# Kernel optimization log

Hardware: AMD Instinct MI355X
Metric: run time of the kernel (lower is better)

The kernel has to match this reference:

```python
import jax, jax.numpy as jnp
import numpy as np

LOG_VAR_Q = 0.0
TEMPERATURE = 0.5


def setup_inputs() -> dict:
    key = jax.random.key(0)
    k1, k2, k3 = jax.random.split(key, 3)
    bs, dim_z, W, H, K = 64, 64, 32, 32, 1024
    x = jax.random.normal(k1, (bs, dim_z, W, H), dtype=jnp.float32)
    codebook = jax.random.normal(k2, (K, dim_z), dtype=jnp.float32)
    log_var_q_scalar = jnp.asarray(0.0, dtype=jnp.float32)
    # pre-sampled standard Gumbel noise for the relaxed categorical
    u = jax.random.uniform(k3, (bs * W * H, K), dtype=jnp.float32,
                           minval=1e-6, maxval=1.0 - 1e-6)
    gumbel_noise = -jnp.log(-jnp.log(u))
    return {"x": x, "codebook": codebook,
            "log_var_q_scalar": log_var_q_scalar,
            "gumbel_noise": gumbel_noise}


def reference(x, codebook, log_var_q_scalar, gumbel_noise):
    bs, dim_z, W, H = x.shape
    # [bs, dim_z, W, H] -> [bs*W*H, dim_z]
    x_flat = jnp.transpose(x, (0, 2, 3, 1)).reshape(-1, dim_z)

    var_q = jnp.exp(jnp.asarray(LOG_VAR_Q, x.dtype)) + jnp.exp(log_var_q_scalar)
    precision_q = 1.0 / jnp.clip(var_q, 1e-10)
    w = 0.5 * precision_q  # scalar weight on squared distances

    sq_x = jnp.sum(x_flat * x_flat, axis=-1, keepdims=True)
    sq_c = jnp.sum(codebook * codebook, axis=-1)
    cross = jnp.einsum('nd,kd->nk', x_flat, codebook)
    logit = -w * (sq_x - 2.0 * cross + sq_c)

    log_probs = jax.nn.log_softmax(logit, axis=-1)
    probs = jnp.exp(log_probs)

    # gumbel-softmax relaxed one-hot encodings
    encodings = jax.nn.softmax((logit + gumbel_noise) / TEMPERATURE, axis=-1)

    quantized = jnp.einsum('nk,kd->nd', encodings, codebook)
    quantized = jnp.transpose(quantized.reshape(bs, W, H, dim_z), (0, 3, 1, 2))

    kld_discrete = jnp.sum(probs * log_probs) / bs
    kld_continuous = jnp.mean(jnp.sum(w * (x - quantized) ** 2, axis=(1, 2, 3)))
    return quantized, kld_discrete + kld_continuous
```

## Files before the change

### kernel.cpp

```cpp
#include <hip/hip_runtime.h>
#include <math.h>

#define K_CB 1024
#define D_Z  64
#define MT   16
#define NTOT 65536
#define NBLK (NTOT / MT)

typedef __attribute__((ext_vector_type(8))) short  s16x8;
typedef __attribute__((ext_vector_type(4))) short  s16x4;
typedef __attribute__((ext_vector_type(4))) float  f32x4;

#define WS_CB16  0
#define WS_CBT16 131072
#define WS_NWSQC 262144
#define WS_PART  266240

__device__ __forceinline__ unsigned short f2b(float f) {
  unsigned int u = __float_as_uint(f);
  u += 0x7fffu + ((u >> 16) & 1u);
  return (unsigned short)(u >> 16);
}

__global__ void vq_prep(const float* __restrict__ cb, const float* __restrict__ lvq,
                        unsigned char* __restrict__ wsb) {
  unsigned short* cb16  = (unsigned short*)(wsb + WS_CB16);
  unsigned short* cbT16 = (unsigned short*)(wsb + WS_CBT16);
  float* nwsqc = (float*)(wsb + WS_NWSQC);
  const float w = 0.5f / fmaxf(1.0f + __expf(lvq[0]), 1e-10f);
  const int tid = threadIdx.x;
  const int k  = blockIdx.x * 16 + (tid >> 4);
  const int d0 = (tid & 15) * 4;
  const f32x4 v = *(const f32x4*)(cb + k * D_Z + d0);
  s16x4 b4;
  #pragma unroll
  for (int i = 0; i < 4; i++) b4[i] = (short)f2b(v[i]);
  *(s16x4*)(cb16 + k * D_Z + d0) = b4;
  #pragma unroll
  for (int i = 0; i < 4; i++) cbT16[(d0 + i) * K_CB + k] = (unsigned short)b4[i];
  float s = v[0]*v[0] + v[1]*v[1] + v[2]*v[2] + v[3]*v[3];
  #pragma unroll
  for (int off = 1; off < 16; off <<= 1) s += __shfl_xor(s, off);
  if ((tid & 15) == 0) nwsqc[k] = -w * s;
}

__global__ __launch_bounds__(256, 3)
void vq_main(const float* __restrict__ x, const float* __restrict__ gum,
             const float* __restrict__ lvq, unsigned char* __restrict__ wsb,
             float* __restrict__ out) {
  __shared__ __align__(16) unsigned short xa[1024];
  __shared__ __align__(16) float xs[MT][68];
  __shared__ __align__(16) float sqcs[K_CB];
  __shared__ __align__(16) unsigned short es[MT][1032];
  __shared__ __align__(16) float pstat[4][MT][4];
  __shared__ __align__(16) float s2p[4][MT];
  __shared__ float kldrow[MT];
  __shared__ float wred[4];

  const int tid  = threadIdx.x;
  const int wv   = tid >> 6;
  const int lane = tid & 63;
  const int m16  = lane & 15;
  const int g    = lane >> 4;

  const int blk  = blockIdx.x;
  const int row0 = blk * MT;
  const int bidx = row0 >> 10;
  const int rem0 = row0 & 1023;

  const float w  = 0.5f / fmaxf(1.0f + __expf(lvq[0]), 1e-10f);
  const float w2 = 2.0f * w;

  const unsigned short* cb16  = (const unsigned short*)(wsb + WS_CB16);
  const unsigned short* cbT16 = (const unsigned short*)(wsb + WS_CBT16);
  const float* nwsqc = (const float*)(wsb + WS_NWSQC);

  {
    const int m = tid & 15, db = tid >> 4;
    #pragma unroll
    for (int i = 0; i < 4; i++) {
      const int d = db + 16 * i;
      const float v = x[((bidx * D_Z + d) << 10) + rem0 + m];
      xs[m][d] = v;
      xa[(d >> 5) * 512 + ((d >> 3) & 3) * 128 + m * 8 + (d & 7)] = f2b(v);
    }
    for (int k = tid; k < K_CB; k += 256) sqcs[k] = nwsqc[k];
  }
  __syncthreads();

  f32x4 acc[16];
  #pragma unroll
  for (int t = 0; t < 16; t++) acc[t] = (f32x4){0.f, 0.f, 0.f, 0.f};
  {
    const s16x8 xb0 = *(const s16x8*)(xa + g * 128 + m16 * 8);
    const s16x8 xb1 = *(const s16x8*)(xa + 512 + g * 128 + m16 * 8);
    const unsigned short* ap = cb16 + (wv * 256 + m16) * D_Z + g * 8;
    #pragma unroll
    for (int t = 0; t < 16; t++) {
      const s16x8 a0 = *(const s16x8*)(ap + t * 1024);
      const s16x8 a1 = *(const s16x8*)(ap + t * 1024 + 32);
      acc[t] = __builtin_amdgcn_mfma_f32_16x16x32_bf16(a0, xb0, acc[t], 0, 0, 0);
      acc[t] = __builtin_amdgcn_mfma_f32_16x16x32_bf16(a1, xb1, acc[t], 0, 0, 0);
    }
  }

  float m1 = -3.4e38f;
  #pragma unroll
  for (int t = 0; t < 16; t++) {
    const f32x4 sc = *(const f32x4*)&sqcs[wv * 256 + t * 16 + g * 4];
    #pragma unroll
    for (int r = 0; r < 4; r++) {
      acc[t][r] = fmaf(w2, acc[t][r], sc[r]);
      m1 = fmaxf(m1, acc[t][r]);
    }
  }
  m1 = fmaxf(m1, __shfl_xor(m1, 16));
  m1 = fmaxf(m1, __shfl_xor(m1, 32));
  float s1 = 0.f, Aa = 0.f;
  #pragma unroll
  for (int t = 0; t < 16; t++) {
    #pragma unroll
    for (int r = 0; r < 4; r++) {
      const float u = acc[t][r] - m1;
      const float e = __expf(u);
      s1 += e;
      Aa = fmaf(u, e, Aa);
    }
  }
  s1 += __shfl_xor(s1, 16); s1 += __shfl_xor(s1, 32);
  Aa += __shfl_xor(Aa, 16); Aa += __shfl_xor(Aa, 32);

  float m2 = -3.4e38f;
  const float* gp = gum + (row0 + m16) * K_CB + wv * 256 + g * 4;
  #pragma unroll
  for (int t = 0; t < 16; t++) {
    const f32x4 gv = __builtin_nontemporal_load((const f32x4*)(gp + t * 16));
    #pragma unroll
    for (int r = 0; r < 4; r++) {
      const float z = 2.0f * (acc[t][r] + gv[r]);
      acc[t][r] = z;
      m2 = fmaxf(m2, z);
    }
  }
  m2 = fmaxf(m2, __shfl_xor(m2, 16));
  m2 = fmaxf(m2, __shfl_xor(m2, 32));
  if (g == 0) {
    pstat[wv][m16][0] = m1; pstat[wv][m16][1] = s1;
    pstat[wv][m16][2] = Aa; pstat[wv][m16][3] = m2;
  }
  __syncthreads();

  float M2 = -3.4e38f;
  {
    float M1 = -3.4e38f;
    f32x4 pw[4];
    #pragma unroll
    for (int q = 0; q < 4; q++) {
      pw[q] = *(const f32x4*)&pstat[q][m16][0];
      M1 = fmaxf(M1, pw[q][0]);
      M2 = fmaxf(M2, pw[q][3]);
    }
    float s1g = 0.f, Ag = 0.f;
    #pragma unroll
    for (int q = 0; q < 4; q++) {
      const float dm = pw[q][0] - M1;
      const float c = __expf(dm);
      s1g += c * pw[q][1];
      Ag = fmaf(c, fmaf(dm, pw[q][1], pw[q][2]), Ag);
    }
    if (tid < 16) kldrow[m16] = Ag / s1g - __logf(s1g);
  }

  float s2 = 0.f;
  #pragma unroll
  for (int t = 0; t < 16; t++) {
    s16x4 ev;
    #pragma unroll
    for (int r = 0; r < 4; r++) {
      const float e = __expf(acc[t][r] - M2);
      s2 += e;
      ev[r] = (short)f2b(e);
    }
    *(s16x4*)&es[m16][wv * 256 + t * 16 + g * 4] = ev;
  }
  s2 += __shfl_xor(s2, 16); s2 += __shfl_xor(s2, 32);
  if (g == 0) s2p[wv][m16] = s2;
  __syncthreads();

  const float inv2 = 1.0f / (s2p[0][m16] + s2p[1][m16] + s2p[2][m16] + s2p[3][m16]);
  f32x4 qacc = (f32x4){0.f, 0.f, 0.f, 0.f};
  {
    const unsigned short* a2p = cbT16 + (wv * 16 + m16) * K_CB + g * 8;
    const unsigned short* b2p = &es[m16][g * 8];
    #pragma unroll
    for (int kc = 0; kc < 32; kc++) {
      const s16x8 a2 = *(const s16x8*)(a2p + kc * 32);
      const s16x8 b2 = *(const s16x8*)(b2p + kc * 32);
      qacc = __builtin_amdgcn_mfma_f32_16x16x32_bf16(a2, b2, qacc, 0, 0, 0);
    }
  }

  float kca = 0.f;
  #pragma unroll
  for (int r = 0; r < 4; r++) {
    const int d = wv * 16 + g * 4 + r;
    const float qv = qacc[r] * inv2;
    __builtin_nontemporal_store(qv, out + ((bidx * D_Z + d) << 10) + rem0 + m16);
    const float dx = xs[m16][d] - qv;
    kca = fmaf(dx, dx, kca);
  }
  #pragma unroll
  for (int off = 1; off < 64; off <<= 1) kca += __shfl_xor(kca, off);
  if (lane == 0) wred[wv] = kca;
  __syncthreads();
  if (tid == 0) {
    float tot = w * (wred[0] + wred[1] + wred[2] + wred[3]);
    #pragma unroll
    for (int i = 0; i < MT; i++) tot += kldrow[i];
    ((float*)(wsb + WS_PART))[blk] = tot;
  }
}

__global__ void vq_reduce(const unsigned char* __restrict__ wsb, float* __restrict__ out) {
  __shared__ float red[256];
  const float* part = (const float*)(wsb + WS_PART);
  const int t = threadIdx.x;
  float s = 0.f;
  for (int i = t; i < NBLK; i += 256) s += part[i];
  red[t] = s;
  __syncthreads();
  for (int st = 128; st > 0; st >>= 1) {
    if (t < st) red[t] += red[t + st];
    __syncthreads();
  }
  if (t == 0) out[NTOT * D_Z] = red[0] * (1.0f / 64.0f);
}

extern "C" void kernel_launch(void* const* d_in, const int* in_sizes, int n_in,
                              void* d_out, int out_size, void* d_ws, size_t ws_size,
                              hipStream_t stream) {
  const float* x   = (const float*)d_in[0];
  const float* cb  = (const float*)d_in[1];
  const float* lvq = (const float*)d_in[2];
  const float* gum = (const float*)d_in[3];
  float* out = (float*)d_out;
  unsigned char* wsb = (unsigned char*)d_ws;

  hipLaunchKernelGGL(vq_prep,   dim3(64),   dim3(256), 0, stream, cb, lvq, wsb);
  hipLaunchKernelGGL(vq_main,   dim3(NBLK), dim3(256), 0, stream, x, gum, lvq, wsb, out);
  hipLaunchKernelGGL(vq_reduce, dim3(1),    dim3(256), 0, stream, wsb, out);
}
```

Baseline: 179.1 us.

## Drop a barrier via per-wave softmax maxima and rescaled quantize partials

Each wave now exponentiates the Gumbel logits against its own local max and writes them to shared memory before the single barrier. The quantize MFMA accumulation is split into four 256-wide chunks, one per wave's slice, each rescaled by exp(m2_wave - M2) when merged, which removes one __syncthreads. It also removes the xs and sqcs shared buffers, reading x and the squared codebook norms directly from global memory. Other changes are software-prefetching codebook fragments across MFMA iterations, issuing Gumbel loads early in staggered groups, and raising the occupancy hint to 4 blocks per CU, which adds register pressure.

```diff
diff --git a/kernel.cpp b/kernel.cpp
--- a/kernel.cpp
+++ b/kernel.cpp
@@ -44,13 +44,13 @@
   if ((tid & 15) == 0) nwsqc[k] = -w * s;
 }
 
-__global__ __launch_bounds__(256, 3)
+#define NTLD(p) __builtin_nontemporal_load((const f32x4*)(p))
+
+__global__ __launch_bounds__(256, 4)
 void vq_main(const float* __restrict__ x, const float* __restrict__ gum,
              const float* __restrict__ lvq, unsigned char* __restrict__ wsb,
              float* __restrict__ out) {
   __shared__ __align__(16) unsigned short xa[1024];
-  __shared__ __align__(16) float xs[MT][68];
-  __shared__ __align__(16) float sqcs[K_CB];
   __shared__ __align__(16) unsigned short es[MT][1032];
   __shared__ __align__(16) float pstat[4][MT][4];
   __shared__ __align__(16) float s2p[4][MT];
@@ -62,7 +62,6 @@
   const int lane = tid & 63;
   const int m16  = lane & 15;
   const int g    = lane >> 4;
-
   const int blk  = blockIdx.x;
   const int row0 = blk * MT;
   const int bidx = row0 >> 10;
@@ -81,10 +80,8 @@
     for (int i = 0; i < 4; i++) {
       const int d = db + 16 * i;
       const float v = x[((bidx * D_Z + d) << 10) + rem0 + m];
-      xs[m][d] = v;
       xa[(d >> 5) * 512 + ((d >> 3) & 3) * 128 + m * 8 + (d & 7)] = f2b(v);
     }
-    for (int k = tid; k < K_CB; k += 256) sqcs[k] = nwsqc[k];
   }
   __syncthreads();
 
@@ -95,19 +92,36 @@
     const s16x8 xb0 = *(const s16x8*)(xa + g * 128 + m16 * 8);
     const s16x8 xb1 = *(const s16x8*)(xa + 512 + g * 128 + m16 * 8);
     const unsigned short* ap = cb16 + (wv * 256 + m16) * D_Z + g * 8;
-    #pragma unroll
-    for (int t = 0; t < 16; t++) {
-      const s16x8 a0 = *(const s16x8*)(ap + t * 1024);
-      const s16x8 a1 = *(const s16x8*)(ap + t * 1024 + 32);
-      acc[t] = __builtin_amdgcn_mfma_f32_16x16x32_bf16(a0, xb0, acc[t], 0, 0, 0);
-      acc[t] = __builtin_amdgcn_mfma_f32_16x16x32_bf16(a1, xb1, acc[t], 0, 0, 0);
-    }
-  }
+    s16x8 c0a = *(const s16x8*)(ap);
+    s16x8 c0b = *(const s16x8*)(ap + 32);
+    s16x8 c1a = *(const s16x8*)(ap + 1024);
+    s16x8 c1b = *(const s16x8*)(ap + 1024 + 32);
+    #pragma unroll
+    for (int c = 0; c < 8; c++) {
+      s16x8 n0a = c0a, n0b = c0b, n1a = c1a, n1b = c1b;
+      if (c < 7) {
+        const unsigned short* np = ap + (2 * c + 2) * 1024;
+        n0a = *(const s16x8*)(np);
+        n0b = *(const s16x8*)(np + 32);
+        n1a = *(const s16x8*)(np + 1024);
+        n1b = *(const s16x8*)(np + 1024 + 32);
+      }
+      acc[2*c]   = __builtin_amdgcn_mfma_f32_16x16x32_bf16(c0a, xb0, acc[2*c],   0, 0, 0);
+      acc[2*c]   = __builtin_amdgcn_mfma_f32_16x16x32_bf16(c0b, xb1, acc[2*c],   0, 0, 0);
+      acc[2*c+1] = __builtin_amdgcn_mfma_f32_16x16x32_bf16(c1a, xb0, acc[2*c+1], 0, 0, 0);
+      acc[2*c+1] = __builtin_amdgcn_mfma_f32_16x16x32_bf16(c1b, xb1, acc[2*c+1], 0, 0, 0);
+      c0a = n0a; c0b = n0b; c1a = n1a; c1b = n1b;
+    }
+  }
+
+  const float* gp = gum + (row0 + m16) * K_CB + wv * 256 + g * 4;
+  f32x4 ga0 = NTLD(gp +   0), ga1 = NTLD(gp +  16), ga2 = NTLD(gp +  32), ga3 = NTLD(gp +  48);
+  f32x4 gb0 = NTLD(gp +  64), gb1 = NTLD(gp +  80), gb2 = NTLD(gp +  96), gb3 = NTLD(gp + 112);
 
   float m1 = -3.4e38f;
   #pragma unroll
   for (int t = 0; t < 16; t++) {
-    const f32x4 sc = *(const f32x4*)&sqcs[wv * 256 + t * 16 + g * 4];
+    const f32x4 sc = *(const f32x4*)(nwsqc + wv * 256 + t * 16 + g * 4);
     #pragma unroll
     for (int r = 0; r < 4; r++) {
       acc[t][r] = fmaf(w2, acc[t][r], sc[r]);
@@ -131,83 +145,99 @@
   Aa += __shfl_xor(Aa, 16); Aa += __shfl_xor(Aa, 32);
 
   float m2 = -3.4e38f;
-  const float* gp = gum + (row0 + m16) * K_CB + wv * 256 + g * 4;
-  #pragma unroll
-  for (int t = 0; t < 16; t++) {
-    const f32x4 gv = __builtin_nontemporal_load((const f32x4*)(gp + t * 16));
-    #pragma unroll
-    for (int r = 0; r < 4; r++) {
-      const float z = 2.0f * (acc[t][r] + gv[r]);
-      acc[t][r] = z;
-      m2 = fmaxf(m2, z);
-    }
-  }
+  #define PROCG(gv, t) { _Pragma("unroll") \
+    for (int r = 0; r < 4; r++) { \
+      const float z = 2.0f * (acc[t][r] + gv[r]); \
+      acc[t][r] = z; m2 = fmaxf(m2, z); } }
+  PROCG(ga0, 0) PROCG(ga1, 1) PROCG(ga2, 2) PROCG(ga3, 3)
+  ga0 = NTLD(gp + 128); ga1 = NTLD(gp + 144); ga2 = NTLD(gp + 160); ga3 = NTLD(gp + 176);
+  PROCG(gb0, 4) PROCG(gb1, 5) PROCG(gb2, 6) PROCG(gb3, 7)
+  gb0 = NTLD(gp + 192); gb1 = NTLD(gp + 208); gb2 = NTLD(gp + 224); gb3 = NTLD(gp + 240);
+  PROCG(ga0,  8) PROCG(ga1,  9) PROCG(ga2, 10) PROCG(ga3, 11)
+  PROCG(gb0, 12) PROCG(gb1, 13) PROCG(gb2, 14) PROCG(gb3, 15)
   m2 = fmaxf(m2, __shfl_xor(m2, 16));
   m2 = fmaxf(m2, __shfl_xor(m2, 32));
   if (g == 0) {
     pstat[wv][m16][0] = m1; pstat[wv][m16][1] = s1;
     pstat[wv][m16][2] = Aa; pstat[wv][m16][3] = m2;
   }
-  __syncthreads();
-
-  float M2 = -3.4e38f;
-  {
-    float M1 = -3.4e38f;
+
+  float s2 = 0.f;
+  #pragma unroll
+  for (int t = 0; t < 16; t++) {
+    s16x4 ev;
+    #pragma unroll
+    for (int r = 0; r < 4; r++) {
+      const float e = __expf(acc[t][r] - m2);
+      s2 += e;
+      ev[r] = (short)f2b(e);
+    }
+    *(s16x4*)&es[m16][wv * 256 + t * 16 + g * 4] = ev;
+  }
+  s2 += __shfl_xor(s2, 16); s2 += __shfl_xor(s2, 32);
+  if (g == 0) s2p[wv][m16] = s2;
+  __syncthreads();
+
+  float cs0, cs1, cs2, cs3, inv2;
+  {
     f32x4 pw[4];
+    float M1 = -3.4e38f, M2 = -3.4e38f;
     #pragma unroll
     for (int q = 0; q < 4; q++) {
       pw[q] = *(const f32x4*)&pstat[q][m16][0];
       M1 = fmaxf(M1, pw[q][0]);
       M2 = fmaxf(M2, pw[q][3]);
     }
-    float s1g = 0.f, Ag = 0.f;
+    float s1g = 0.f, Ag = 0.f, s2g = 0.f, csv[4];
     #pragma unroll
     for (int q = 0; q < 4; q++) {
       const float dm = pw[q][0] - M1;
-      const float c = __expf(dm);
+      const float c  = __expf(dm);
       s1g += c * pw[q][1];
       Ag = fmaf(c, fmaf(dm, pw[q][1], pw[q][2]), Ag);
-    }
+      const float c2 = __expf(pw[q][3] - M2);
+      csv[q] = c2;
+      s2g = fmaf(c2, s2p[q][m16], s2g);
+    }
+    cs0 = csv[0]; cs1 = csv[1]; cs2 = csv[2]; cs3 = csv[3];
+    inv2 = 1.0f / s2g;
     if (tid < 16) kldrow[m16] = Ag / s1g - __logf(s1g);
   }
 
-  float s2 = 0.f;
-  #pragma unroll
-  for (int t = 0; t < 16; t++) {
-    s16x4 ev;
-    #pragma unroll
-    for (int r = 0; r < 4; r++) {
-      const float e = __expf(acc[t][r] - M2);
-      s2 += e;
-      ev[r] = (short)f2b(e);
-    }
-    *(s16x4*)&es[m16][wv * 256 + t * 16 + g * 4] = ev;
-  }
-  s2 += __shfl_xor(s2, 16); s2 += __shfl_xor(s2, 32);
-  if (g == 0) s2p[wv][m16] = s2;
-  __syncthreads();
-
-  const float inv2 = 1.0f / (s2p[0][m16] + s2p[1][m16] + s2p[2][m16] + s2p[3][m16]);
-  f32x4 qacc = (f32x4){0.f, 0.f, 0.f, 0.f};
+  float qt0 = 0.f, qt1 = 0.f, qt2 = 0.f, qt3 = 0.f;
   {
     const unsigned short* a2p = cbT16 + (wv * 16 + m16) * K_CB + g * 8;
     const unsigned short* b2p = &es[m16][g * 8];
-    #pragma unroll
-    for (int kc = 0; kc < 32; kc++) {
-      const s16x8 a2 = *(const s16x8*)(a2p + kc * 32);
-      const s16x8 b2 = *(const s16x8*)(b2p + kc * 32);
-      qacc = __builtin_amdgcn_mfma_f32_16x16x32_bf16(a2, b2, qacc, 0, 0, 0);
+    const float csa[4] = {cs0, cs1, cs2, cs3};
+    #pragma unroll
+    for (int b = 0; b < 4; b++) {
+      f32x4 qa = (f32x4){0.f, 0.f, 0.f, 0.f};
+      #pragma unroll
+      for (int kc = 0; kc < 8; kc++) {
+        const int kk = b * 8 + kc;
+        const s16x8 a2 = *(const s16x8*)(a2p + kk * 32);
+        const s16x8 b2 = *(const s16x8*)(b2p + kk * 32);
+        qa = __builtin_amdgcn_mfma_f32_16x16x32_bf16(a2, b2, qa, 0, 0, 0);
+      }
+      qt0 = fmaf(csa[b], qa[0], qt0);
+      qt1 = fmaf(csa[b], qa[1], qt1);
+      qt2 = fmaf(csa[b], qa[2], qt2);
+      qt3 = fmaf(csa[b], qa[3], qt3);
     }
   }
 
   float kca = 0.f;
-  #pragma unroll
-  for (int r = 0; r < 4; r++) {
-    const int d = wv * 16 + g * 4 + r;
-    const float qv = qacc[r] * inv2;
-    __builtin_nontemporal_store(qv, out + ((bidx * D_Z + d) << 10) + rem0 + m16);
-    const float dx = xs[m16][d] - qv;
-    kca = fmaf(dx, dx, kca);
+  {
+    const float qv[4] = {qt0 * inv2, qt1 * inv2, qt2 * inv2, qt3 * inv2};
+    #pragma unroll
+    for (int r = 0; r < 4; r++) {
+      const int d = wv * 16 + g * 4 + r;
+      const int off = ((bidx * D_Z + d) << 10) + rem0 + m16;
+      const float xv = x[off];
+      __builtin_nontemporal_store(qv[r], out + off);
+      const float dx = xv - qv[r];
+      kca = fmaf(dx, dx, kca);
+    }
   }
   #pragma unroll
   for (int off = 1; off < 64; off <<= 1) kca += __shfl_xor(kca, off);
```

Result: slower. 192.8 us (+7.7%).

## Stage Gumbel noise into LDS with async double-buffered loads and remap codebook tiles

Applied to the files above, without the earlier changes.

Gumbel noise rows are now streamed through a double-buffered, XOR-swizzled LDS staging area using global_load_lds, with explicit waitcnt and barriers so the loads overlap the first GEMM and softmax. The codebook tiles are interleaved across waves with software-prefetched operands, and the block index is swizzled. The squared-norm table and the x copy in LDS are dropped: norms are read from global memory and x is reloaded at the end, freeing shared memory for the staging buffers. The cost is more barriers, hand-written wait counts that are fragile, and extra global reads.

```diff
diff --git a/kernel.cpp b/kernel.cpp
--- a/kernel.cpp
+++ b/kernel.cpp
@@ -10,6 +10,9 @@
 typedef __attribute__((ext_vector_type(8))) short  s16x8;
 typedef __attribute__((ext_vector_type(4))) short  s16x4;
 typedef __attribute__((ext_vector_type(4))) float  f32x4;
+
+typedef __attribute__((address_space(1))) const unsigned char gu8;
+typedef __attribute__((address_space(3))) unsigned char lu8;
 
 #define WS_CB16  0
 #define WS_CBT16 131072
@@ -49,11 +52,11 @@
              const float* __restrict__ lvq, unsigned char* __restrict__ wsb,
              float* __restrict__ out) {
   __shared__ __align__(16) unsigned short xa[1024];
-  __shared__ __align__(16) float xs[MT][68];
-  __shared__ __align__(16) float sqcs[K_CB];
   __shared__ __align__(16) unsigned short es[MT][1032];
+  __shared__ __align__(16) float stg[2][2048];
   __shared__ __align__(16) float pstat[4][MT][4];
   __shared__ __align__(16) float s2p[4][MT];
+  __shared__ float m2p[4][MT];
   __shared__ float kldrow[MT];
   __shared__ float wred[4];
 
@@ -62,8 +65,8 @@
   const int lane = tid & 63;
   const int m16  = lane & 15;
   const int g    = lane >> 4;
-
-  const int blk  = blockIdx.x;
+  const int bid  = blockIdx.x;
+  const int blk  = ((bid & 7) << 9) | (bid >> 3);
   const int row0 = blk * MT;
   const int bidx = row0 >> 10;
   const int rem0 = row0 & 1023;
@@ -81,12 +84,24 @@
     for (int i = 0; i < 4; i++) {
       const int d = db + 16 * i;
       const float v = x[((bidx * D_Z + d) << 10) + rem0 + m];
-      xs[m][d] = v;
       xa[(d >> 5) * 512 + ((d >> 3) & 3) * 128 + m * 8 + (d & 7)] = f2b(v);
     }
-    for (int k = tid; k < K_CB; k += 256) sqcs[k] = nwsqc[k];
-  }
-  __syncthreads();
+  }
+  __syncthreads();
+
+  auto STAGE = [&](int c, int buf) {
+    #pragma unroll
+    for (int s = 0; s < 2; s++) {
+      const int k = (wv << 1) + s;
+      const int r = (k << 1) + (lane >> 5);
+      const gu8* src = (gu8*)((const unsigned char*)gum +
+          (((size_t)(row0 + r)) << 12) + (c << 9) + (((lane & 31) ^ (r & 7)) << 4));
+      lu8* dst = (lu8*)((unsigned char*)&stg[buf][0] + (k << 10));
+      __builtin_amdgcn_global_load_lds(src, dst, 16, 0, 0);
+    }
+  };
+  STAGE(0, 0);
+  STAGE(1, 1);
 
   f32x4 acc[16];
   #pragma unroll
@@ -94,20 +109,33 @@
   {
     const s16x8 xb0 = *(const s16x8*)(xa + g * 128 + m16 * 8);
     const s16x8 xb1 = *(const s16x8*)(xa + 512 + g * 128 + m16 * 8);
-    const unsigned short* ap = cb16 + (wv * 256 + m16) * D_Z + g * 8;
-    #pragma unroll
-    for (int t = 0; t < 16; t++) {
-      const s16x8 a0 = *(const s16x8*)(ap + t * 1024);
-      const s16x8 a1 = *(const s16x8*)(ap + t * 1024 + 32);
-      acc[t] = __builtin_amdgcn_mfma_f32_16x16x32_bf16(a0, xb0, acc[t], 0, 0, 0);
-      acc[t] = __builtin_amdgcn_mfma_f32_16x16x32_bf16(a1, xb1, acc[t], 0, 0, 0);
+    const unsigned short* ap = cb16 + (wv * 16 + m16) * D_Z + g * 8;
+    s16x8 c0a = *(const s16x8*)(ap);
+    s16x8 c0b = *(const s16x8*)(ap + 32);
+    s16x8 c1a = *(const s16x8*)(ap + 4096);
+    s16x8 c1b = *(const s16x8*)(ap + 4096 + 32);
+    #pragma unroll
+    for (int cp = 0; cp < 8; cp++) {
+      s16x8 n0a = c0a, n0b = c0b, n1a = c1a, n1b = c1b;
+      if (cp < 7) {
+        const unsigned short* np = ap + (2 * cp + 2) * 4096;
+        n0a = *(const s16x8*)(np);
+        n0b = *(const s16x8*)(np + 32);
+        n1a = *(const s16x8*)(np + 4096);
+        n1b = *(const s16x8*)(np + 4096 + 32);
+      }
+      acc[2*cp]   = __builtin_amdgcn_mfma_f32_16x16x32_bf16(c0a, xb0, acc[2*cp],   0, 0, 0);
+      acc[2*cp]   = __builtin_amdgcn_mfma_f32_16x16x32_bf16(c0b, xb1, acc[2*cp],   0, 0, 0);
+      acc[2*cp+1] = __builtin_amdgcn_mfma_f32_16x16x32_bf16(c1a, xb0, acc[2*cp+1], 0, 0, 0);
+      acc[2*cp+1] = __builtin_amdgcn_mfma_f32_16x16x32_bf16(c1b, xb1, acc[2*cp+1], 0, 0, 0);
+      c0a = n0a; c0b = n0b; c1a = n1a; c1b = n1b;
     }
   }
 
   float m1 = -3.4e38f;
   #pragma unroll
   for (int t = 0; t < 16; t++) {
-    const f32x4 sc = *(const f32x4*)&sqcs[wv * 256 + t * 16 + g * 4];
+    const f32x4 sc = *(const f32x4*)(nwsqc + t * 64 + wv * 16 + g * 4);
     #pragma unroll
     for (int r = 0; r < 4; r++) {
       acc[t][r] = fmaf(w2, acc[t][r], sc[r]);
@@ -129,59 +157,72 @@
   }
   s1 += __shfl_xor(s1, 16); s1 += __shfl_xor(s1, 32);
   Aa += __shfl_xor(Aa, 16); Aa += __shfl_xor(Aa, 32);
+  if (g == 0) {
+    pstat[wv][m16][0] = m1; pstat[wv][m16][1] = s1; pstat[wv][m16][2] = Aa;
+  }
 
   float m2 = -3.4e38f;
-  const float* gp = gum + (row0 + m16) * K_CB + wv * 256 + g * 4;
-  #pragma unroll
-  for (int t = 0; t < 16; t++) {
-    const f32x4 gv = __builtin_nontemporal_load((const f32x4*)(gp + t * 16));
-    #pragma unroll
-    for (int r = 0; r < 4; r++) {
-      const float z = 2.0f * (acc[t][r] + gv[r]);
-      acc[t][r] = z;
-      m2 = fmaxf(m2, z);
-    }
-  }
+  #pragma unroll
+  for (int c = 0; c < 8; c++) {
+    if (c < 7) { asm volatile("s_waitcnt vmcnt(2)" ::: "memory"); }
+    else       { asm volatile("s_waitcnt vmcnt(0)" ::: "memory"); }
+    __builtin_amdgcn_s_barrier();
+    __builtin_amdgcn_sched_barrier(0);
+    const unsigned char* bp = (const unsigned char*)&stg[c & 1][0];
+    #pragma unroll
+    for (int h = 0; h < 2; h++) {
+      const int i = (c << 1) + h;
+      const f32x4 gv = *(const f32x4*)(bp + (m16 << 9) +
+                        ((((h << 4) + (wv << 2) + g) ^ (m16 & 7)) << 4));
+      #pragma unroll
+      for (int r = 0; r < 4; r++) {
+        const float z = 2.0f * (acc[i][r] + gv[r]);
+        acc[i][r] = z;
+        m2 = fmaxf(m2, z);
+      }
+    }
+    asm volatile("s_waitcnt lgkmcnt(0)" ::: "memory");
+    __builtin_amdgcn_sched_barrier(0);
+    __builtin_amdgcn_s_barrier();
+    if (c < 6) STAGE(c + 2, c & 1);
+  }
+
   m2 = fmaxf(m2, __shfl_xor(m2, 16));
   m2 = fmaxf(m2, __shfl_xor(m2, 32));
-  if (g == 0) {
-    pstat[wv][m16][0] = m1; pstat[wv][m16][1] = s1;
-    pstat[wv][m16][2] = Aa; pstat[wv][m16][3] = m2;
-  }
-  __syncthreads();
-
-  float M2 = -3.4e38f;
-  {
+  if (g == 0) m2p[wv][m16] = m2;
+  __syncthreads();
+  const float M2 = fmaxf(fmaxf(m2p[0][m16], m2p[1][m16]),
+                         fmaxf(m2p[2][m16], m2p[3][m16]));
+  if (tid < 16) {
     float M1 = -3.4e38f;
     f32x4 pw[4];
     #pragma unroll
     for (int q = 0; q < 4; q++) {
-      pw[q] = *(const f32x4*)&pstat[q][m16][0];
+      pw[q] = *(const f32x4*)&pstat[q][tid][0];
       M1 = fmaxf(M1, pw[q][0]);
-      M2 = fmaxf(M2, pw[q][3]);
     }
     float s1g = 0.f, Ag = 0.f;
     #pragma unroll
     for (int q = 0; q < 4; q++) {
       const float dm = pw[q][0] - M1;
-      const float c = __expf(dm);
-      s1g += c * pw[q][1];
-      Ag = fmaf(c, fmaf(dm, pw[q][1], pw[q][2]), Ag);
-    }
-    if (tid < 16) kldrow[m16] = Ag / s1g - __logf(s1g);
+      const float cc = __expf(dm);
+      s1g += cc * pw[q][1];
+      Ag = fmaf(cc, fmaf(dm, pw[q][1], pw[q][2]), Ag);
+    }
+    kldrow[tid] = Ag / s1g - __logf(s1g);
   }
 
   float s2 = 0.f;
   #pragma unroll
-  for (int t = 0; t < 16; t++) {
+  for (int i = 0; i < 16; i++) {
     s16x4 ev;
     #pragma unroll
     for (int r = 0; r < 4; r++) {
-      const float e = __expf(acc[t][r] - M2);
+      const float e = __expf(acc[i][r] - M2);
       s2 += e;
       ev[r] = (short)f2b(e);
     }
-    *(s16x4*)&es[m16][wv * 256 + t * 16 + g * 4] = ev;
+    *(s16x4*)&es[m16][((4 * i + wv) << 4) + (g << 2)] = ev;
   }
   s2 += __shfl_xor(s2, 16); s2 += __shfl_xor(s2, 32);
   if (g == 0) s2p[wv][m16] = s2;
@@ -204,9 +245,11 @@
   #pragma unroll
   for (int r = 0; r < 4; r++) {
     const int d = wv * 16 + g * 4 + r;
+    const int off = ((bidx * D_Z + d) << 10) + rem0 + m16;
     const float qv = qacc[r] * inv2;
-    __builtin_nontemporal_store(qv, out + ((bidx * D_Z + d) << 10) + rem0 + m16);
-    const float dx = xs[m16][d] - qv;
+    const float xv = x[off];
+    out[off] = qv;
+    const float dx = xv - qv;
     kca = fmaf(dx, dx, kca);
   }
   #pragma unroll
```

New measurement: 170.6 us. 1.05x faster.

## Retile VQ kernel to 32-row blocks with 32x32 MFMA and swizzled LDS

Applied to the files above, without the earlier changes.

Doubles rows per block to 32 and uses 512 threads (8 waves, 128 codebook entries each). The distance GEMM moves from 16x16x32 to 32x32x16 MFMA, and the x and encoding tiles in LDS use XOR swizzling to avoid bank conflicts. It also remaps block IDs across the grid, loads Gumbel noise in two batches, reads codebook norms directly from global memory, and re-reads x from global memory instead of keeping an fp32 copy. The goal is better reuse of the codebook per block and fewer LDS conflicts. The cost is higher register pressure and a larger LDS footprint (64KB for es), which may limit occupancy.

```diff
diff --git a/kernel.cpp b/kernel.cpp
--- a/kernel.cpp
+++ b/kernel.cpp
@@ -3,13 +3,14 @@
 
 #define K_CB 1024
 #define D_Z  64
-#define MT   16
+#define MT   32
 #define NTOT 65536
 #define NBLK (NTOT / MT)
 
-typedef __attribute__((ext_vector_type(8))) short  s16x8;
-typedef __attribute__((ext_vector_type(4))) short  s16x4;
-typedef __attribute__((ext_vector_type(4))) float  f32x4;
+typedef __attribute__((ext_vector_type(8)))  short s16x8;
+typedef __attribute__((ext_vector_type(4)))  short s16x4;
+typedef __attribute__((ext_vector_type(4)))  float f32x4;
+typedef __attribute__((ext_vector_type(16))) float f32x16;
 
 #define WS_CB16  0
 #define WS_CBT16 131072
@@ -44,158 +45,200 @@
   if ((tid & 15) == 0) nwsqc[k] = -w * s;
 }
 
-__global__ __launch_bounds__(256, 3)
+__global__ __launch_bounds__(512, 4)
 void vq_main(const float* __restrict__ x, const float* __restrict__ gum,
              const float* __restrict__ lvq, unsigned char* __restrict__ wsb,
              float* __restrict__ out) {
-  __shared__ __align__(16) unsigned short xa[1024];
-  __shared__ __align__(16) float xs[MT][68];
-  __shared__ __align__(16) float sqcs[K_CB];
-  __shared__ __align__(16) unsigned short es[MT][1032];
-  __shared__ __align__(16) float pstat[4][MT][4];
-  __shared__ __align__(16) float s2p[4][MT];
+  __shared__ __align__(16) unsigned short xa[MT * D_Z];
+  __shared__ __align__(16) unsigned short es[MT * K_CB];
+  __shared__ __align__(16) float stats[8][MT][4];
+  __shared__ __align__(16) float s2s[8][MT];
   __shared__ float kldrow[MT];
-  __shared__ float wred[4];
+  __shared__ float wred[8];
 
   const int tid  = threadIdx.x;
-  const int wv   = tid >> 6;
+  const int w    = tid >> 6;
   const int lane = tid & 63;
-  const int m16  = lane & 15;
-  const int g    = lane >> 4;
-
-  const int blk  = blockIdx.x;
+  const int m32  = lane & 31;
+  const int hi   = lane >> 5;
+  const int bid  = blockIdx.x;
+  const int blk  = ((bid & 7) << 8) | (bid >> 3);
   const int row0 = blk * MT;
   const int bidx = row0 >> 10;
   const int rem0 = row0 & 1023;
-
-  const float w  = 0.5f / fmaxf(1.0f + __expf(lvq[0]), 1e-10f);
-  const float w2 = 2.0f * w;
+  const int kw0  = w << 7;
+
+  const float wq = 0.5f / fmaxf(1.0f + __expf(lvq[0]), 1e-10f);
+  const float w2 = 2.0f * wq;
 
   const unsigned short* cb16  = (const unsigned short*)(wsb + WS_CB16);
   const unsigned short* cbT16 = (const unsigned short*)(wsb + WS_CBT16);
   const float* nwsqc = (const float*)(wsb + WS_NWSQC);
 
   {
-    const int m = tid & 15, db = tid >> 4;
+    const int m = tid & 31, dg = tid >> 5;
     #pragma unroll
     for (int i = 0; i < 4; i++) {
-      const int d = db + 16 * i;
+      const int d = dg + 16 * i;
       const float v = x[((bidx * D_Z + d) << 10) + rem0 + m];
-      xs[m][d] = v;
-      xa[(d >> 5) * 512 + ((d >> 3) & 3) * 128 + m * 8 + (d & 7)] = f2b(v);
-    }
-    for (int k = tid; k < K_CB; k += 256) sqcs[k] = nwsqc[k];
-  }
-  __syncthreads();
-
-  f32x4 acc[16];
-  #pragma unroll
-  for (int t = 0; t < 16; t++) acc[t] = (f32x4){0.f, 0.f, 0.f, 0.f};
+      xa[(m * D_Z + d) ^ ((m & 7) << 3)] = f2b(v);
+    }
+  }
+  __syncthreads();
+
+  f32x16 acc[4];
+  #pragma unroll
+  for (int t = 0; t < 4; t++)
+    #pragma unroll
+    for (int r = 0; r < 16; r++) acc[t][r] = 0.f;
   {
-    const s16x8 xb0 = *(const s16x8*)(xa + g * 128 + m16 * 8);
-    const s16x8 xb1 = *(const s16x8*)(xa + 512 + g * 128 + m16 * 8);
-    const unsigned short* ap = cb16 + (wv * 256 + m16) * D_Z + g * 8;
-    #pragma unroll
-    for (int t = 0; t < 16; t++) {
-      const s16x8 a0 = *(const s16x8*)(ap + t * 1024);
-      const s16x8 a1 = *(const s16x8*)(ap + t * 1024 + 32);
-      acc[t] = __builtin_amdgcn_mfma_f32_16x16x32_bf16(a0, xb0, acc[t], 0, 0, 0);
-      acc[t] = __builtin_amdgcn_mfma_f32_16x16x32_bf16(a1, xb1, acc[t], 0, 0, 0);
+    s16x8 bx[4];
+    #pragma unroll
+    for (int kb = 0; kb < 4; kb++) {
+      const int byteoff = (m32 * 128 + kb * 32 + hi * 16) ^ ((m32 & 7) << 4);
+      bx[kb] = *(const s16x8*)((const unsigned char*)xa + byteoff);
+    }
+    #pragma unroll
+    for (int t = 0; t < 4; t++) {
+      const unsigned short* ap = cb16 + (kw0 + t * 32 + m32) * D_Z + hi * 8;
+      #pragma unroll
+      for (int kb = 0; kb < 4; kb++) {
+        const s16x8 a = *(const s16x8*)(ap + kb * 16);
+        acc[t] = __builtin_amdgcn_mfma_f32_32x32x16_bf16(a, bx[kb], acc[t], 0, 0, 0);
+      }
     }
   }
 
   float m1 = -3.4e38f;
   #pragma unroll
-  for (int t = 0; t < 16; t++) {
-    const f32x4 sc = *(const f32x4*)&sqcs[wv * 256 + t * 16 + g * 4];
-    #pragma unroll
-    for (int r = 0; r < 4; r++) {
-      acc[t][r] = fmaf(w2, acc[t][r], sc[r]);
-      m1 = fmaxf(m1, acc[t][r]);
-    }
-  }
-  m1 = fmaxf(m1, __shfl_xor(m1, 16));
+  for (int t = 0; t < 4; t++) {
+    #pragma unroll
+    for (int q = 0; q < 4; q++) {
+      const f32x4 nw = *(const f32x4*)(nwsqc + kw0 + t * 32 + q * 8 + hi * 4);
+      #pragma unroll
+      for (int i = 0; i < 4; i++) {
+        acc[t][q * 4 + i] = fmaf(w2, acc[t][q * 4 + i], nw[i]);
+        m1 = fmaxf(m1, acc[t][q * 4 + i]);
+      }
+    }
+  }
   m1 = fmaxf(m1, __shfl_xor(m1, 32));
+
+  const float* gp = gum + ((size_t)(row0 + m32) << 10) + kw0 + hi * 4;
+  f32x4 gA[8];
+  #pragma unroll
+  for (int u = 0; u < 8; u++)
+    gA[u] = *(const f32x4*)(gp + (u >> 2) * 32 + (u & 3) * 8);
+
   float s1 = 0.f, Aa = 0.f;
   #pragma unroll
-  for (int t = 0; t < 16; t++) {
-    #pragma unroll
-    for (int r = 0; r < 4; r++) {
+  for (int t = 0; t < 4; t++) {
+    #pragma unroll
+    for (int r = 0; r < 16; r++) {
       const float u = acc[t][r] - m1;
       const float e = __expf(u);
       s1 += e;
       Aa = fmaf(u, e, Aa);
     }
   }
-  s1 += __shfl_xor(s1, 16); s1 += __shfl_xor(s1, 32);
-  Aa += __shfl_xor(Aa, 16); Aa += __shfl_xor(Aa, 32);
+  s1 += __shfl_xor(s1, 32);
+  Aa += __shfl_xor(Aa, 32);
 
   float m2 = -3.4e38f;
-  const float* gp = gum + (row0 + m16) * K_CB + wv * 256 + g * 4;
-  #pragma unroll
-  for (int t = 0; t < 16; t++) {
-    const f32x4 gv = __builtin_nontemporal_load((const f32x4*)(gp + t * 16));
-    #pragma unroll
-    for (int r = 0; r < 4; r++) {
-      const float z = 2.0f * (acc[t][r] + gv[r]);
-      acc[t][r] = z;
+  #pragma unroll
+  for (int u = 0; u < 8; u++) {
+    const int t = u >> 2, q = u & 3;
+    #pragma unroll
+    for (int i = 0; i < 4; i++) {
+      const float z = 2.0f * (acc[t][q * 4 + i] + gA[u][i]);
+      acc[t][q * 4 + i] = z;
       m2 = fmaxf(m2, z);
     }
   }
-  m2 = fmaxf(m2, __shfl_xor(m2, 16));
+  f32x4 gB[8];
+  #pragma unroll
+  for (int u = 0; u < 8; u++)
+    gB[u] = *(const f32x4*)(gp + 64 + (u >> 2) * 32 + (u & 3) * 8);
+  #pragma unroll
+  for (int u = 0; u < 8; u++) {
+    const int t = 2 + (u >> 2), q = u & 3;
+    #pragma unroll
+    for (int i = 0; i < 4; i++) {
+      const float z = 2.0f * (acc[t][q * 4 + i] + gB[u][i]);
+      acc[t][q * 4 + i] = z;
+      m2 = fmaxf(m2, z);
+    }
+  }
   m2 = fmaxf(m2, __shfl_xor(m2, 32));
-  if (g == 0) {
-    pstat[wv][m16][0] = m1; pstat[wv][m16][1] = s1;
-    pstat[wv][m16][2] = Aa; pstat[wv][m16][3] = m2;
+  if (hi == 0) {
+    f32x4 st = {m1, s1, Aa, m2};
+    *(f32x4*)&stats[w][m32][0] = st;
   }
   __syncthreads();
 
   float M2 = -3.4e38f;
   {
-    float M1 = -3.4e38f;
-    f32x4 pw[4];
+    f32x4 st[8];
+    #pragma unroll
+    for (int q = 0; q < 8; q++) {
+      st[q] = *(const f32x4*)&stats[q][m32][0];
+      M2 = fmaxf(M2, st[q][3]);
+    }
+    if (w == 0) {
+      float M1 = -3.4e38f;
+      #pragma unroll
+      for (int q = 0; q < 8; q++) M1 = fmaxf(M1, st[q][0]);
+      float s1g = 0.f, Ag = 0.f;
+      #pragma unroll
+      for (int q = 0; q < 8; q++) {
+        const float dm = st[q][0] - M1;
+        const float c  = __expf(dm);
+        s1g += c * st[q][1];
+        Ag = fmaf(c, fmaf(dm, st[q][1], st[q][2]), Ag);
+      }
+      if (hi == 0) kldrow[m32] = Ag / s1g - __logf(s1g);
+    }
+  }
+
+  float s2 = 0.f;
+  #pragma unroll
+  for (int t = 0; t < 4; t++) {
     #pragma unroll
     for (int q = 0; q < 4; q++) {
-      pw[q] = *(const f32x4*)&pstat[q][m16][0];
-      M1 = fmaxf(M1, pw[q][0]);
-      M2 = fmaxf(M2, pw[q][3]);
-    }
-    float s1g = 0.f, Ag = 0.f;
-    #pragma unroll
-    for (int q = 0; q < 4; q++) {
-      const float dm = pw[q][0] - M1;
-      const float c = __expf(dm);
-      s1g += c * pw[q][1];
-      Ag = fmaf(c, fmaf(dm, pw[q][1], pw[q][2]), Ag);
-    }
-    if (tid < 16) kldrow[m16] = Ag / s1g - __logf(s1g);
-  }
-
-  float s2 = 0.f;
-  #pragma unroll
-  for (int t = 0; t < 16; t++) {
-    s16x4 ev;
-    #pragma unroll
-    for (int r = 0; r < 4; r++) {
-      const float e = __expf(acc[t][r] - M2);
-      s2 += e;
-      ev[r] = (short)f2b(e);
-    }
-    *(s16x4*)&es[m16][wv * 256 + t * 16 + g * 4] = ev;
-  }
-  s2 += __shfl_xor(s2, 16); s2 += __shfl_xor(s2, 32);
-  if (g == 0) s2p[wv][m16] = s2;
-  __syncthreads();
-
-  const float inv2 = 1.0f / (s2p[0][m16] + s2p[1][m16] + s2p[2][m16] + s2p[3][m16]);
+      float e[4];
+      #pragma unroll
+      for (int i = 0; i < 4; i++) {
+        e[i] = __expf(acc[t][q * 4 + i] - M2);
+        s2 += e[i];
+      }
+      const unsigned int p0 = (unsigned int)f2b(e[0]) | ((unsigned int)f2b(e[1]) << 16);
+      const unsigned int p1 = (unsigned int)f2b(e[2]) | ((unsigned int)f2b(e[3]) << 16);
+      const unsigned long long pk = (unsigned long long)p0 | ((unsigned long long)p1 << 32);
+      const int byteoff = (m32 * 2048 + (kw0 + t * 32 + q * 8 + hi * 4) * 2) ^ ((m32 & 7) << 4);
+      *(unsigned long long*)((unsigned char*)es + byteoff) = pk;
+    }
+  }
+  s2 += __shfl_xor(s2, 32);
+  if (hi == 0) s2s[w][m32] = s2;
+  __syncthreads();
+
+  const int m16 = lane & 15, g = lane >> 4;
+  const int db = w >> 1, mb = w & 1;
+  const int mrow = mb * 16 + m16;
+  float s2g = 0.f;
+  #pragma unroll
+  for (int q = 0; q < 8; q++) s2g += s2s[q][mrow];
+  const float inv2 = 1.0f / s2g;
+
   f32x4 qacc = (f32x4){0.f, 0.f, 0.f, 0.f};
   {
-    const unsigned short* a2p = cbT16 + (wv * 16 + m16) * K_CB + g * 8;
-    const unsigned short* b2p = &es[m16][g * 8];
+    const unsigned short* a2p = cbT16 + (db * 16 + m16) * K_CB + g * 8;
+    const unsigned char* esb = (const unsigned char*)es;
     #pragma unroll
     for (int kc = 0; kc < 32; kc++) {
       const s16x8 a2 = *(const s16x8*)(a2p + kc * 32);
-      const s16x8 b2 = *(const s16x8*)(b2p + kc * 32);
+      const int byteoff = (mrow * 2048 + kc * 64 + g * 16) ^ ((m16 & 7) << 4);
+      const s16x8 b2 = *(const s16x8*)(esb + byteoff);
       qacc = __builtin_amdgcn_mfma_f32_16x16x32_bf16(a2, b2, qacc, 0, 0, 0);
     }
   }
@@ -203,18 +246,23 @@
   float kca = 0.f;
   #pragma unroll
   for (int r = 0; r < 4; r++) {
-    const int d = wv * 16 + g * 4 + r;
+    const int d = db * 16 + g * 4 + r;
+    const int off = ((bidx * D_Z + d) << 10) + rem0 + mrow;
     const float qv = qacc[r] * inv2;
-    __builtin_nontemporal_store(qv, out + ((bidx * D_Z + d) << 10) + rem0 + m16);
-    const float dx = xs[m16][d] - qv;
+    const float xv = x[off];
+    out[off] = qv;
+    const float dx = xv - qv;
     kca = fmaf(dx, dx, kca);
   }
   #pragma unroll
   for (int off = 1; off < 64; off <<= 1) kca += __shfl_xor(kca, off);
-  if (lane == 0) wred[wv] = kca;
+  if (lane == 0) wred[w] = kca;
   __syncthreads();
   if (tid == 0) {
-    float tot = w * (wred[0] + wred[1] + wred[2] + wred[3]);
+    float tot = 0.f;
+    #pragma unroll
+    for (int q = 0; q < 8; q++) tot += wred[q];
+    tot *= wq;
     #pragma unroll
     for (int i = 0; i < MT; i++) tot += kldrow[i];
     ((float*)(wsb + WS_PART))[blk] = tot;
@@ -247,6 +295,6 @@
   unsigned char* wsb = (unsigned char*)d_ws;
 
   hipLaunchKernelGGL(vq_prep,   dim3(64),   dim3(256), 0, stream, cb, lvq, wsb);
-  hipLaunchKernelGGL(vq_main,   dim3(NBLK), dim3(256), 0, stream, x, gum, lvq, wsb, out);
+  hipLaunchKernelGGL(vq_main,   dim3(NBLK), dim3(512), 0, stream, x, gum, lvq, wsb, out);
   hipLaunchKernelGGL(vq_reduce, dim3(1),    dim3(256), 0, stream, wsb, out);
 }
```

New measurement: 160.5 us. 1.12x faster.
